# Kernel tuning notes

Measured on AMD Instinct MI355X. Metric: run time of the kernel, lower is better.

## Reference

```python
import jax, jax.numpy as jnp
import numpy as np

DIM = 1024
NUM_HEADS = 16
HEAD_DIM = DIM // NUM_HEADS
SCALE = HEAD_DIM ** -0.5


def rotate_half(x):
    x1, x2 = jnp.split(x, 2, axis=-1)
    return jnp.concatenate((-x2, x1), axis=-1)


def setup_inputs() -> dict:
    key = jax.random.key(0)
    ks = jax.random.split(key, 8)
    B, N = 2, 2048
    x = jax.random.normal(ks[0], (B, N, DIM), dtype=jnp.float32)
    # RoPE tables, broadcast over batch and heads
    pos = jnp.arange(N, dtype=jnp.float32)[:, None]
    inv_freq = 1.0 / (10000.0 ** (jnp.arange(0, HEAD_DIM, 2, dtype=jnp.float32) / HEAD_DIM))
    ang = pos * inv_freq[None, :]                       # [N, HEAD_DIM/2]
    ang = jnp.concatenate([ang, ang], axis=-1)          # [N, HEAD_DIM]
    rope_cos = jnp.cos(ang)[None, None]                 # [1,1,N,HEAD_DIM]
    rope_sin = jnp.sin(ang)[None, None]
    s = DIM ** -0.5
    qkv_w = jax.random.normal(ks[1], (3 * DIM, DIM), dtype=jnp.float32) * s
    qkv_b = jnp.zeros((3 * DIM,), dtype=jnp.float32)
    proj_w = jax.random.normal(ks[2], (DIM, DIM), dtype=jnp.float32) * s
    proj_b = jnp.zeros((DIM,), dtype=jnp.float32)
    return {"x": x, "rope_cos": rope_cos, "rope_sin": rope_sin,
            "qkv_w": qkv_w, "qkv_b": qkv_b, "proj_w": proj_w, "proj_b": proj_b}


def reference(x, rope_cos, rope_sin, qkv_w, qkv_b, proj_w, proj_b):
    B, N, C = x.shape
    H, D = NUM_HEADS, HEAD_DIM
    qkv = x @ qkv_w.T + qkv_b                            # [B,N,3C]
    qkv = qkv.reshape(B, N, 3, H, D).transpose(2, 0, 3, 1, 4)  # [3,B,H,N,D]
    q, k, v = qkv[0], qkv[1], qkv[2]
    # RoPE on q, k
    q = q * rope_cos + rotate_half(q) * rope_sin
    k = k * rope_cos + rotate_half(k) * rope_sin
    # scaled dot-product attention
    scores = jnp.einsum('bhnd,bhmd->bhnm', q, k) * SCALE
    attn = jax.nn.softmax(scores, axis=-1)
    out = jnp.einsum('bhnm,bhmd->bhnd', attn, v)         # [B,H,N,D]
    out = out.transpose(0, 2, 1, 3).reshape(B, N, C)
    return out @ proj_w.T + proj_b
```

## Files before the change

### kernel.cpp

```cpp
#include <hip/hip_runtime.h>
#include <hip/hip_bf16.h>

#define NUM_HEADS 16
#define HEAD_DIM 64
#define DIM 1024
#define NTOK 2048
#define MTOT 4096

typedef __attribute__((ext_vector_type(8))) short bf16x8;
typedef __attribute__((ext_vector_type(4))) float f32x4;

__device__ __forceinline__ unsigned short f2bf(float f) {
    union { __hip_bfloat16 h; unsigned short u; } c;
    c.h = __float2bfloat16(f);
    return c.u;
}

__device__ __forceinline__ void gload16(const unsigned short* g, unsigned short* l) {
    __builtin_amdgcn_global_load_lds(
        (const __attribute__((address_space(1))) void*)g,
        (__attribute__((address_space(3))) void*)l, 16, 0, 0);
}

__global__ __launch_bounds__(256) void k_conv(const float* __restrict__ src,
                                              unsigned short* __restrict__ dst, int n)
{
    int i = (blockIdx.x * 256 + threadIdx.x) * 8;
    if (i >= n) return;
    float4 a = *(const float4*)(src + i);
    float4 b = *(const float4*)(src + i + 4);
    union { unsigned short us[8]; uint4 u4; } p;
    p.us[0] = f2bf(a.x); p.us[1] = f2bf(a.y); p.us[2] = f2bf(a.z); p.us[3] = f2bf(a.w);
    p.us[4] = f2bf(b.x); p.us[5] = f2bf(b.y); p.us[6] = f2bf(b.z); p.us[7] = f2bf(b.w);
    *(uint4*)(dst + i) = p.u4;
}

__global__ __launch_bounds__(256) void k_gemm_qkv(
    const unsigned short* __restrict__ xb, const unsigned short* __restrict__ wb,
    const float* __restrict__ bias, const float* __restrict__ rcos,
    const float* __restrict__ rsin,
    unsigned short* __restrict__ qb, unsigned short* __restrict__ kb,
    unsigned short* __restrict__ vtb)
{
    __shared__ __align__(16) unsigned char smem[34816];
    unsigned short* As = (unsigned short*)smem;
    unsigned short* Bs = (unsigned short*)(smem + 16384);

    const int tid  = threadIdx.x;
    const int lane = tid & 63;
    const int wid  = tid >> 6;
    const int lr   = lane & 15;
    const int g    = lane >> 4;
    const int wm   = (wid >> 1) * 64;
    const int wn   = (wid & 1) * 64;
    const int m0   = blockIdx.x * 128;
    const int n0   = blockIdx.y * 128;

    f32x4 acc[4][4];
    #pragma unroll
    for (int i = 0; i < 4; ++i)
        #pragma unroll
        for (int j = 0; j < 4; ++j) acc[i][j] = (f32x4){0.f, 0.f, 0.f, 0.f};

    for (int k0 = 0; k0 < DIM; k0 += 64) {
        #pragma unroll
        for (int it = 0; it < 4; ++it) {
            int p   = tid + it * 256;
            int row = p >> 3;
            int c   = (p & 7) ^ (row & 7);
            gload16(xb + (size_t)(m0 + row) * DIM + k0 + c*8, As + p*8);
            gload16(wb + (size_t)(n0 + row) * DIM + k0 + c*8, Bs + p*8);
        }
        __syncthreads();
        #pragma unroll
        for (int kk = 0; kk < 2; ++kk) {
            bf16x8 af[4], bfr[4];
            #pragma unroll
            for (int i = 0; i < 4; ++i) {
                int row = wm + i*16 + lr;
                af[i] = *(const bf16x8*)(As + row*64 + (((kk*4 + g) ^ (row & 7)) << 3));
            }
            #pragma unroll
            for (int j = 0; j < 4; ++j) {
                int row = wn + j*16 + lr;
                bfr[j] = *(const bf16x8*)(Bs + row*64 + (((kk*4 + g) ^ (row & 7)) << 3));
            }
            #pragma unroll
            for (int i = 0; i < 4; ++i)
                #pragma unroll
                for (int j = 0; j < 4; ++j)
                    acc[i][j] = __builtin_amdgcn_mfma_f32_16x16x32_bf16(af[i], bfr[j], acc[i][j], 0, 0, 0);
        }
        __syncthreads();
    }

    const int sect = n0 >> 10;
    float bq[4];
    #pragma unroll
    for (int j = 0; j < 4; ++j) bq[j] = bias[n0 + wn + j*16 + lr];

    if (sect < 2) {
        unsigned short* dst = sect ? kb : qb;
        const float sc = sect ? 1.0f : 0.125f * 1.44269504088896f;
        const int h = ((n0 & 1023) + wn) >> 6;
        #pragma unroll
        for (int i = 0; i < 4; ++i) {
            #pragma unroll
            for (int v = 0; v < 4; ++v) {
                int gm = m0 + wm + i*16 + g*4 + v;
                int b  = gm >> 11, n = gm & 2047;
                size_t base = ((size_t)(b*NUM_HEADS + h) * NTOK + n) << 6;
                #pragma unroll
                for (int j = 0; j < 4; ++j) {
                    int d = j*16 + lr;
                    float val = acc[i][j][v] + bq[j];
                    float vp  = acc[i][j^2][v] + bq[j^2];
                    float rot = (j < 2) ? -vp : vp;
                    float c = rcos[n*64 + d], s = rsin[n*64 + d];
                    dst[base + d] = f2bf((val * c + rot * s) * sc);
                }
            }
        }
    } else {
        unsigned short (*vt)[136] = (unsigned short (*)[136])smem;
        __syncthreads();
        #pragma unroll
        for (int i = 0; i < 4; ++i)
            #pragma unroll
            for (int j = 0; j < 4; ++j)
                #pragma unroll
                for (int v = 0; v < 4; ++v) {
                    int row = wm + i*16 + g*4 + v;
                    int c   = wn + j*16 + lr;
                    vt[c][row] = f2bf(acc[i][j][v] + bq[j]);
                }
        __syncthreads();
        const int b = m0 >> 11;
        const int nbase = m0 & 2047;
        #pragma unroll
        for (int it = 0; it < 8; ++it) {
            int c   = (tid >> 4) + it * 16;
            int sc2 = (n0 & 1023) + c;
            int hh  = sc2 >> 6, d = sc2 & 63;
            int nloc = (tid & 15) * 8;
            uint4 val = *(uint4*)&vt[c][nloc];
            *(uint4*)(vtb + ((size_t)(b*NUM_HEADS + hh) * HEAD_DIM + d) * NTOK + nbase + nloc) = val;
        }
    }
}

__global__ __launch_bounds__(256, 4) void k_attn(
    const unsigned short* __restrict__ qb, const unsigned short* __restrict__ kb,
    const unsigned short* __restrict__ vtb, unsigned short* __restrict__ attnb)
{
    __shared__ __align__(16) unsigned short kbuf[2][4096];
    __shared__ __align__(16) unsigned short vbuf[2][4096];
    __shared__ __align__(16) unsigned short pbuf[4][1024];

    const int tid  = threadIdx.x;
    const int lane = tid & 63;
    const int w    = tid >> 6;
    const int g    = lane >> 4;
    const int lr   = lane & 15;
    const int q0   = blockIdx.x * 64;
    const int bh   = blockIdx.y;
    const int b    = bh >> 4, h = bh & 15;

    const unsigned short* kbase = kb  + (size_t)bh * NTOK * 64;
    const unsigned short* vbase = vtb + (size_t)bh * HEAD_DIM * NTOK;

    bf16x8 qa[2];
    {
        size_t qrow = ((size_t)bh * NTOK + q0 + w*16 + lr) * 64;
        #pragma unroll
        for (int kk = 0; kk < 2; ++kk)
            qa[kk] = *(const bf16x8*)(qb + qrow + kk*32 + g*8);
    }

    f32x4 o[4];
    float m_[4], lsum[4];
    #pragma unroll
    for (int fd = 0; fd < 4; ++fd) o[fd] = (f32x4){0.f, 0.f, 0.f, 0.f};
    #pragma unroll
    for (int v = 0; v < 4; ++v) { m_[v] = -1e30f; lsum[v] = 0.f; }

    #pragma unroll
    for (int hp = 0; hp < 2; ++hp) {
        int p   = tid + hp * 256;
        int row = p >> 3;
        int c   = (p & 7) ^ (row & 7);
        gload16(kbase + (size_t)row*64 + c*8, &kbuf[0][p*8]);
        gload16(vbase + (size_t)row*NTOK + c*8, &vbuf[0][p*8]);
    }
    __syncthreads();

    int cur = 0;
    for (int t = 0; t < NTOK/64; ++t) {
        if (t < NTOK/64 - 1) {
            int kvn = (t + 1) * 64;
            #pragma unroll
            for (int hp = 0; hp < 2; ++hp) {
                int p   = tid + hp * 256;
                int row = p >> 3;
                int c   = (p & 7) ^ (row & 7);
                gload16(kbase + (size_t)(kvn + row)*64 + c*8, &kbuf[cur^1][p*8]);
                gload16(vbase + (size_t)row*NTOK + kvn + c*8, &vbuf[cur^1][p*8]);
            }
        }

        f32x4 s[4];
        #pragma unroll
        for (int fn = 0; fn < 4; ++fn) s[fn] = (f32x4){0.f, 0.f, 0.f, 0.f};
        #pragma unroll
        for (int kk = 0; kk < 2; ++kk) {
            bf16x8 kf[4];
            #pragma unroll
            for (int fn = 0; fn < 4; ++fn) {
                int row = fn*16 + lr;
                kf[fn] = *(const bf16x8*)&kbuf[cur][row*64 + (((kk*4 + g) ^ (row & 7)) << 3)];
            }
            #pragma unroll
            for (int fn = 0; fn < 4; ++fn)
                s[fn] = __builtin_amdgcn_mfma_f32_16x16x32_bf16(qa[kk], kf[fn], s[fn], 0, 0, 0);
        }

        float lmax[4];
        int need = 0;
        #pragma unroll
        for (int v = 0; v < 4; ++v) {
            lmax[v] = fmaxf(fmaxf(s[0][v], s[1][v]), fmaxf(s[2][v], s[3][v]));
            need |= (lmax[v] > m_[v] + 8.f);
        }
        if (__any(need)) {
            #pragma unroll
            for (int v = 0; v < 4; ++v) {
                float mx = lmax[v];
                mx = fmaxf(mx, __shfl_xor(mx, 1));
                mx = fmaxf(mx, __shfl_xor(mx, 2));
                mx = fmaxf(mx, __shfl_xor(mx, 4));
                mx = fmaxf(mx, __shfl_xor(mx, 8));
                float mn  = fmaxf(m_[v], mx);
                float scl = __builtin_amdgcn_exp2f(m_[v] - mn);
                m_[v] = mn;
                lsum[v] *= scl;
                #pragma unroll
                for (int fd = 0; fd < 4; ++fd) o[fd][v] *= scl;
            }
        }

        unsigned short* pw = pbuf[w];
        #pragma unroll
        for (int fn = 0; fn < 4; ++fn)
            #pragma unroll
            for (int v = 0; v < 4; ++v) {
                float p = __builtin_amdgcn_exp2f(s[fn][v] - m_[v]);
                lsum[v] += p;
                int row = g*4 + v;
                int col = fn*16 + lr;
                pw[row*64 + (((col >> 3) ^ (row & 7)) << 3) + (col & 7)] = f2bf(p);
            }

        #pragma unroll
        for (int kk = 0; kk < 2; ++kk) {
            bf16x8 pa, vf[4];
            pa = *(const bf16x8*)&pw[lr*64 + (((kk*4 + g) ^ (lr & 7)) << 3)];
            #pragma unroll
            for (int fd = 0; fd < 4; ++fd) {
                int row = fd*16 + lr;
                vf[fd] = *(const bf16x8*)&vbuf[cur][row*64 + (((kk*4 + g) ^ (row & 7)) << 3)];
            }
            #pragma unroll
            for (int fd = 0; fd < 4; ++fd)
                o[fd] = __builtin_amdgcn_mfma_f32_16x16x32_bf16(pa, vf[fd], o[fd], 0, 0, 0);
        }
        __syncthreads();
        cur ^= 1;
    }

    #pragma unroll
    for (int v = 0; v < 4; ++v) {
        float l = lsum[v];
        l += __shfl_xor(l, 1);
        l += __shfl_xor(l, 2);
        l += __shfl_xor(l, 4);
        l += __shfl_xor(l, 8);
        lsum[v] = 1.0f / l;
    }
    #pragma unroll
    for (int fd = 0; fd < 4; ++fd)
        #pragma unroll
        for (int v = 0; v < 4; ++v) {
            int n = q0 + w*16 + g*4 + v;
            attnb[((size_t)(b*NTOK + n)) * DIM + h*HEAD_DIM + fd*16 + lr] =
                f2bf(o[fd][v] * lsum[v]);
        }
}

__global__ __launch_bounds__(256) void k_proj(
    const unsigned short* __restrict__ a, const unsigned short* __restrict__ wb,
    const float* __restrict__ bias, float* __restrict__ out)
{
    __shared__ __align__(16) unsigned short As[8192];
    __shared__ __align__(16) unsigned short Bs[8192];

    const int tid  = threadIdx.x;
    const int lane = tid & 63;
    const int wid  = tid >> 6;
    const int lr   = lane & 15;
    const int g    = lane >> 4;
    const int wm   = (wid >> 1) * 64;
    const int wn   = (wid & 1) * 64;
    const int m0   = blockIdx.x * 128;
    const int n0   = blockIdx.y * 128;

    f32x4 acc[4][4];
    #pragma unroll
    for (int i = 0; i < 4; ++i)
        #pragma unroll
        for (int j = 0; j < 4; ++j) acc[i][j] = (f32x4){0.f, 0.f, 0.f, 0.f};

    for (int k0 = 0; k0 < DIM; k0 += 64) {
        #pragma unroll
        for (int it = 0; it < 4; ++it) {
            int p   = tid + it * 256;
            int row = p >> 3;
            int c   = (p & 7) ^ (row & 7);
            gload16(a  + (size_t)(m0 + row) * DIM + k0 + c*8, As + p*8);
            gload16(wb + (size_t)(n0 + row) * DIM + k0 + c*8, Bs + p*8);
        }
        __syncthreads();
        #pragma unroll
        for (int kk = 0; kk < 2; ++kk) {
            bf16x8 af[4], bfr[4];
            #pragma unroll
            for (int i = 0; i < 4; ++i) {
                int row = wm + i*16 + lr;
                af[i] = *(const bf16x8*)(As + row*64 + (((kk*4 + g) ^ (row & 7)) << 3));
            }
            #pragma unroll
            for (int j = 0; j < 4; ++j) {
                int row = wn + j*16 + lr;
                bfr[j] = *(const bf16x8*)(Bs + row*64 + (((kk*4 + g) ^ (row & 7)) << 3));
            }
            #pragma unroll
            for (int i = 0; i < 4; ++i)
                #pragma unroll
                for (int j = 0; j < 4; ++j)
                    acc[i][j] = __builtin_amdgcn_mfma_f32_16x16x32_bf16(af[i], bfr[j], acc[i][j], 0, 0, 0);
        }
        __syncthreads();
    }

    #pragma unroll
    for (int i = 0; i < 4; ++i)
        #pragma unroll
        for (int j = 0; j < 4; ++j)
            #pragma unroll
            for (int v = 0; v < 4; ++v) {
                int row = m0 + wm + i*16 + g*4 + v;
                int col = n0 + wn + j*16 + lr;
                out[(size_t)row * DIM + col] = acc[i][j][v] + bias[col];
            }
}

extern "C" void kernel_launch(void* const* d_in, const int* in_sizes, int n_in,
                              void* d_out, int out_size, void* d_ws, size_t ws_size,
                              hipStream_t stream)
{
    const float* x      = (const float*)d_in[0];
    const float* rcos   = (const float*)d_in[1];
    const float* rsin   = (const float*)d_in[2];
    const float* qkv_w  = (const float*)d_in[3];
    const float* qkv_b  = (const float*)d_in[4];
    const float* proj_w = (const float*)d_in[5];
    const float* proj_b = (const float*)d_in[6];
    float* out = (float*)d_out;

    const size_t BUF = (size_t)2 * NUM_HEADS * NTOK * HEAD_DIM;
    unsigned short* qb    = (unsigned short*)d_ws;
    unsigned short* kb    = qb + BUF;
    unsigned short* vtb   = kb + BUF;
    unsigned short* attnb = vtb + BUF;
    unsigned short* xbf   = attnb + BUF;
    unsigned short* wqkvb = xbf + (size_t)MTOT * DIM;
    unsigned short* wprjb = wqkvb + (size_t)3 * DIM * DIM;

    k_conv<<<dim3((MTOT*DIM)/2048), 256, 0, stream>>>(x, xbf, MTOT*DIM);
    k_conv<<<dim3((3*DIM*DIM)/2048), 256, 0, stream>>>(qkv_w, wqkvb, 3*DIM*DIM);
    k_conv<<<dim3((DIM*DIM)/2048), 256, 0, stream>>>(proj_w, wprjb, DIM*DIM);

    k_gemm_qkv<<<dim3(32, 24), 256, 0, stream>>>(xbf, wqkvb, qkv_b, rcos, rsin, qb, kb, vtb);
    k_attn<<<dim3(NTOK/64, 32), 256, 0, stream>>>(qb, kb, vtb, attnb);
    k_proj<<<dim3(32, 8), 256, 0, stream>>>(attnb, wprjb, proj_b, out);
}
```

Measured before the change: 142.5 us.

## Merge conversion launches and restructure attention loop with precomputed LDS offsets

The three fp32-to-bf16 conversion kernels are merged into one launch that picks its source and destination per block. The attention inner loop is unrolled by two with compile-time buffer offsets, precomputed swizzled LDS byte offsets and incrementing global pointers, which cuts per-iteration address arithmetic. It also raises wave priority around the MFMA groups with s_setprio. The changes trade some register pressure for fewer integer ops and one fewer pair of kernel launches.

```diff
diff --git a/kernel.cpp b/kernel.cpp
--- a/kernel.cpp
+++ b/kernel.cpp
@@ -22,17 +22,24 @@
         (__attribute__((address_space(3))) void*)l, 16, 0, 0);
 }
 
-__global__ __launch_bounds__(256) void k_conv(const float* __restrict__ src,
-                                              unsigned short* __restrict__ dst, int n)
+__global__ __launch_bounds__(256) void k_conv3(
+    const float* __restrict__ s0, unsigned short* __restrict__ d0, int n0,
+    const float* __restrict__ s1, unsigned short* __restrict__ d1, int n1,
+    const float* __restrict__ s2, unsigned short* __restrict__ d2, int n2)
 {
-    int i = (blockIdx.x * 256 + threadIdx.x) * 8;
-    if (i >= n) return;
-    float4 a = *(const float4*)(src + i);
-    float4 b = *(const float4*)(src + i + 4);
+    int blk = blockIdx.x;
+    int b0 = n0 >> 11, b1 = n1 >> 11;
+    const float* s; unsigned short* d; int i;
+    if (blk < b0)            { s = s0; d = d0; i = blk; }
+    else if (blk < b0 + b1)  { s = s1; d = d1; i = blk - b0; }
+    else                     { s = s2; d = d2; i = blk - b0 - b1; }
+    int idx = (i * 256 + threadIdx.x) * 8;
+    float4 a = *(const float4*)(s + idx);
+    float4 b = *(const float4*)(s + idx + 4);
     union { unsigned short us[8]; uint4 u4; } p;
     p.us[0] = f2bf(a.x); p.us[1] = f2bf(a.y); p.us[2] = f2bf(a.z); p.us[3] = f2bf(a.w);
     p.us[4] = f2bf(b.x); p.us[5] = f2bf(b.y); p.us[6] = f2bf(b.z); p.us[7] = f2bf(b.w);
-    *(uint4*)(dst + i) = p.u4;
+    *(uint4*)(d + idx) = p.u4;
 }
 
 __global__ __launch_bounds__(256) void k_gemm_qkv(
@@ -153,9 +160,7 @@
     const unsigned short* __restrict__ qb, const unsigned short* __restrict__ kb,
     const unsigned short* __restrict__ vtb, unsigned short* __restrict__ attnb)
 {
-    __shared__ __align__(16) unsigned short kbuf[2][4096];
-    __shared__ __align__(16) unsigned short vbuf[2][4096];
-    __shared__ __align__(16) unsigned short pbuf[4][1024];
+    __shared__ __align__(16) char sb[40960];
 
     const int tid  = threadIdx.x;
     const int lane = tid & 63;
@@ -166,8 +171,43 @@
     const int bh   = blockIdx.y;
     const int b    = bh >> 4, h = bh & 15;
 
-    const unsigned short* kbase = kb  + (size_t)bh * NTOK * 64;
-    const unsigned short* vbase = vtb + (size_t)bh * HEAD_DIM * NTOK;
+    int kfoff[2][4], vfoff[2][4], paoff[2], pwoff[4][4];
+    #pragma unroll
+    for (int kk = 0; kk < 2; ++kk) {
+        #pragma unroll
+        for (int fn = 0; fn < 4; ++fn) {
+            int row = fn*16 + lr;
+            int sw  = ((kk*4 + g) ^ (row & 7)) << 4;
+            kfoff[kk][fn] = row*128 + sw;
+            vfoff[kk][fn] = 16384 + row*128 + sw;
+        }
+        paoff[kk] = 32768 + w*2048 + lr*128 + (((kk*4 + g) ^ (lr & 7)) << 4);
+    }
+    #pragma unroll
+    for (int fn = 0; fn < 4; ++fn)
+        #pragma unroll
+        for (int v = 0; v < 4; ++v) {
+            int row = g*4 + v, col = fn*16 + lr;
+            pwoff[fn][v] = 32768 + w*2048 + row*128 + (((col >> 3) ^ (row & 7)) << 4) + (col & 7)*2;
+        }
+
+    const unsigned short* gk[2];
+    const unsigned short* gv[2];
+    char* dk[2]; char* dv[2];
+    {
+        const unsigned short* kbase = kb  + (size_t)bh * NTOK * 64;
+        const unsigned short* vbase = vtb + (size_t)bh * HEAD_DIM * NTOK;
+        #pragma unroll
+        for (int hp = 0; hp < 2; ++hp) {
+            int p   = tid + hp * 256;
+            int row = p >> 3;
+            int c   = (p & 7) ^ (row & 7);
+            gk[hp] = kbase + row*64 + c*8;
+            gv[hp] = vbase + (size_t)row*NTOK + c*8;
+            dk[hp] = sb + p*16;
+            dv[hp] = sb + 16384 + p*16;
+        }
+    }
 
     bf16x8 qa[2];
     {
@@ -186,96 +226,89 @@
 
     #pragma unroll
     for (int hp = 0; hp < 2; ++hp) {
-        int p   = tid + hp * 256;
-        int row = p >> 3;
-        int c   = (p & 7) ^ (row & 7);
-        gload16(kbase + (size_t)row*64 + c*8, &kbuf[0][p*8]);
-        gload16(vbase + (size_t)row*NTOK + c*8, &vbuf[0][p*8]);
+        gload16(gk[hp], (unsigned short*)dk[hp]);
+        gload16(gv[hp], (unsigned short*)dv[hp]);
+        gk[hp] += 4096; gv[hp] += 64;
     }
     __syncthreads();
 
-    int cur = 0;
-    for (int t = 0; t < NTOK/64; ++t) {
-        if (t < NTOK/64 - 1) {
-            int kvn = (t + 1) * 64;
-            #pragma unroll
-            for (int hp = 0; hp < 2; ++hp) {
-                int p   = tid + hp * 256;
-                int row = p >> 3;
-                int c   = (p & 7) ^ (row & 7);
-                gload16(kbase + (size_t)(kvn + row)*64 + c*8, &kbuf[cur^1][p*8]);
-                gload16(vbase + (size_t)row*NTOK + kvn + c*8, &vbuf[cur^1][p*8]);
-            }
-        }
-
-        f32x4 s[4];
-        #pragma unroll
-        for (int fn = 0; fn < 4; ++fn) s[fn] = (f32x4){0.f, 0.f, 0.f, 0.f};
-        #pragma unroll
-        for (int kk = 0; kk < 2; ++kk) {
-            bf16x8 kf[4];
-            #pragma unroll
-            for (int fn = 0; fn < 4; ++fn) {
-                int row = fn*16 + lr;
-                kf[fn] = *(const bf16x8*)&kbuf[cur][row*64 + (((kk*4 + g) ^ (row & 7)) << 3)];
-            }
-            #pragma unroll
-            for (int fn = 0; fn < 4; ++fn)
-                s[fn] = __builtin_amdgcn_mfma_f32_16x16x32_bf16(qa[kk], kf[fn], s[fn], 0, 0, 0);
-        }
-
-        float lmax[4];
-        int need = 0;
-        #pragma unroll
-        for (int v = 0; v < 4; ++v) {
-            lmax[v] = fmaxf(fmaxf(s[0][v], s[1][v]), fmaxf(s[2][v], s[3][v]));
-            need |= (lmax[v] > m_[v] + 8.f);
-        }
-        if (__any(need)) {
-            #pragma unroll
-            for (int v = 0; v < 4; ++v) {
-                float mx = lmax[v];
-                mx = fmaxf(mx, __shfl_xor(mx, 1));
-                mx = fmaxf(mx, __shfl_xor(mx, 2));
-                mx = fmaxf(mx, __shfl_xor(mx, 4));
-                mx = fmaxf(mx, __shfl_xor(mx, 8));
-                float mn  = fmaxf(m_[v], mx);
-                float scl = __builtin_amdgcn_exp2f(m_[v] - mn);
-                m_[v] = mn;
-                lsum[v] *= scl;
-                #pragma unroll
-                for (int fd = 0; fd < 4; ++fd) o[fd][v] *= scl;
-            }
-        }
-
-        unsigned short* pw = pbuf[w];
-        #pragma unroll
-        for (int fn = 0; fn < 4; ++fn)
-            #pragma unroll
-            for (int v = 0; v < 4; ++v) {
-                float p = __builtin_amdgcn_exp2f(s[fn][v] - m_[v]);
-                lsum[v] += p;
-                int row = g*4 + v;
-                int col = fn*16 + lr;
-                pw[row*64 + (((col >> 3) ^ (row & 7)) << 3) + (col & 7)] = f2bf(p);
-            }
-
-        #pragma unroll
-        for (int kk = 0; kk < 2; ++kk) {
-            bf16x8 pa, vf[4];
-            pa = *(const bf16x8*)&pw[lr*64 + (((kk*4 + g) ^ (lr & 7)) << 3)];
-            #pragma unroll
-            for (int fd = 0; fd < 4; ++fd) {
-                int row = fd*16 + lr;
-                vf[fd] = *(const bf16x8*)&vbuf[cur][row*64 + (((kk*4 + g) ^ (row & 7)) << 3)];
-            }
-            #pragma unroll
-            for (int fd = 0; fd < 4; ++fd)
-                o[fd] = __builtin_amdgcn_mfma_f32_16x16x32_bf16(pa, vf[fd], o[fd], 0, 0, 0);
-        }
-        __syncthreads();
-        cur ^= 1;
-    }
+#define ATTN_ITER(X, DO_STAGE)                                                   \
+    {                                                                            \
+        if (DO_STAGE) {                                                          \
+            _Pragma("unroll")                                                    \
+            for (int hp = 0; hp < 2; ++hp) {                                     \
+                gload16(gk[hp], (unsigned short*)(dk[hp] + ((X) ^ 8192)));       \
+                gload16(gv[hp], (unsigned short*)(dv[hp] + ((X) ^ 8192)));       \
+                gk[hp] += 4096; gv[hp] += 64;                                    \
+            }                                                                    \
+        }                                                                        \
+        f32x4 s_[4];                                                             \
+        _Pragma("unroll")                                                        \
+        for (int fn = 0; fn < 4; ++fn) s_[fn] = (f32x4){0.f, 0.f, 0.f, 0.f};     \
+        _Pragma("unroll")                                                        \
+        for (int kk = 0; kk < 2; ++kk) {                                         \
+            bf16x8 kf[4];                                                        \
+            _Pragma("unroll")                                                    \
+            for (int fn = 0; fn < 4; ++fn)                                       \
+                kf[fn] = *(const bf16x8*)(sb + kfoff[kk][fn] + (X));             \
+            __builtin_amdgcn_s_setprio(1);                                       \
+            _Pragma("unroll")                                                    \
+            for (int fn = 0; fn < 4; ++fn)                                       \
+                s_[fn] = __builtin_amdgcn_mfma_f32_16x16x32_bf16(qa[kk], kf[fn], s_[fn], 0, 0, 0); \
+            __builtin_amdgcn_s_setprio(0);                                       \
+        }                                                                        \
+        float lmax[4]; int need = 0;                                             \
+        _Pragma("unroll")                                                        \
+        for (int v = 0; v < 4; ++v) {                                            \
+            lmax[v] = fmaxf(fmaxf(fmaxf(s_[0][v], s_[1][v]), s_[2][v]), s_[3][v]); \
+            need |= (lmax[v] > m_[v] + 8.f);                                     \
+        }                                                                        \
+        if (__any(need)) {                                                       \
+            _Pragma("unroll")                                                    \
+            for (int v = 0; v < 4; ++v) {                                        \
+                float mx = lmax[v];                                              \
+                mx = fmaxf(mx, __shfl_xor(mx, 1));                               \
+                mx = fmaxf(mx, __shfl_xor(mx, 2));                               \
+                mx = fmaxf(mx, __shfl_xor(mx, 4));                               \
+                mx = fmaxf(mx, __shfl_xor(mx, 8));                               \
+                float mn  = fmaxf(m_[v], mx);                                    \
+                float scl = __builtin_amdgcn_exp2f(m_[v] - mn);                  \
+                m_[v] = mn;                                                      \
+                lsum[v] *= scl;                                                  \
+                _Pragma("unroll")                                                \
+                for (int fd = 0; fd < 4; ++fd) o[fd][v] *= scl;                  \
+            }                                                                    \
+        }                                                                        \
+        _Pragma("unroll")                                                        \
+        for (int fn = 0; fn < 4; ++fn)                                           \
+            _Pragma("unroll")                                                    \
+            for (int v = 0; v < 4; ++v) {                                        \
+                float p = __builtin_amdgcn_exp2f(s_[fn][v] - m_[v]);             \
+                lsum[v] += p;                                                    \
+                *(unsigned short*)(sb + pwoff[fn][v]) = f2bf(p);                 \
+            }                                                                    \
+        _Pragma("unroll")                                                        \
+        for (int kk = 0; kk < 2; ++kk) {                                         \
+            bf16x8 pa = *(const bf16x8*)(sb + paoff[kk]);                        \
+            bf16x8 vf[4];                                                        \
+            _Pragma("unroll")                                                    \
+            for (int fd = 0; fd < 4; ++fd)                                       \
+                vf[fd] = *(const bf16x8*)(sb + vfoff[kk][fd] + (X));             \
+            __builtin_amdgcn_s_setprio(1);                                       \
+            _Pragma("unroll")                                                    \
+            for (int fd = 0; fd < 4; ++fd)                                       \
+                o[fd] = __builtin_amdgcn_mfma_f32_16x16x32_bf16(pa, vf[fd], o[fd], 0, 0, 0); \
+            __builtin_amdgcn_s_setprio(0);                                       \
+        }                                                                        \
+        __syncthreads();                                                         \
+    }
+
+    #pragma unroll 1
+    for (int t = 0; t < NTOK/64; t += 2) {
+        ATTN_ITER(0,    true);
+        ATTN_ITER(8192, (t + 2 < NTOK/64));
+    }
+#undef ATTN_ITER
 
     #pragma unroll
     for (int v = 0; v < 4; ++v) {
@@ -385,9 +418,9 @@
     unsigned short* wqkvb = xbf + (size_t)MTOT * DIM;
     unsigned short* wprjb = wqkvb + (size_t)3 * DIM * DIM;
 
-    k_conv<<<dim3((MTOT*DIM)/2048), 256, 0, stream>>>(x, xbf, MTOT*DIM);
-    k_conv<<<dim3((3*DIM*DIM)/2048), 256, 0, stream>>>(qkv_w, wqkvb, 3*DIM*DIM);
-    k_conv<<<dim3((DIM*DIM)/2048), 256, 0, stream>>>(proj_w, wprjb, DIM*DIM);
+    const int n0 = MTOT * DIM, n1 = 3 * DIM * DIM, n2 = DIM * DIM;
+    k_conv3<<<dim3((n0 + n1 + n2) / 2048), 256, 0, stream>>>(
+        x, xbf, n0, qkv_w, wqkvb, n1, proj_w, wprjb, n2);
 
     k_gemm_qkv<<<dim3(32, 24), 256, 0, stream>>>(xbf, wqkvb, qkv_b, rcos, rsin, qb, kb, vtb);
     k_attn<<<dim3(NTOK/64, 32), 256, 0, stream>>>(qb, kb, vtb, attnb);
```

New measurement: 135.7 us. -4.8%, faster.
